# Kernel tuning notes

Measured on AMD Instinct MI355X. Metric: run time of the kernel, lower is better.

Reference implementation:

```python
import jax, jax.numpy as jnp
import numpy as np
from jax.scipy.special import ndtri

BLOCK_SIZE = 32
NF5_OFFSET = 0.9677083  # QLoRA-style tail quantile offset


def _nf5_table():
    # 32-level NormalFloat-5 table: 16 negative levels, zero, 15 positive levels,
    # taken from standard-normal quantiles and normalized so endpoints hit -1 / +1.
    neg = ndtri(jnp.linspace(1.0 - NF5_OFFSET, 0.5, 17))[:-1]   # 16 negative quantiles
    pos = ndtri(jnp.linspace(0.5, NF5_OFFSET, 16))[1:]          # 15 positive quantiles
    neg = neg / (-neg[0])
    pos = pos / pos[-1]
    return jnp.concatenate([neg, jnp.zeros((1,)), pos]).astype(jnp.float32)


def nf5_quantize(x, block_size, table, boundaries):
    # Block-wise NF5 quantization with power-of-2 scales along the last dim.
    shp = x.shape
    xb = x.reshape(-1, block_size)                               # [nblocks, B]
    amax = jnp.max(jnp.abs(xb), axis=1, keepdims=True)
    scale = jnp.exp2(jnp.ceil(jnp.log2(jnp.maximum(amax, 1e-12))))  # power-of-2 scale
    n = xb / scale                                               # normalized to [-1, 1]
    idx = jnp.searchsorted(boundaries, n)                        # nearest-level index
    q = table[idx] * scale                                       # fused dequant
    return q.reshape(shp)


def setup_inputs() -> dict:
    key = jax.random.key(0)
    k1, k2, k3 = jax.random.split(key, 3)
    B, S, Din, Dout = 8, 4096, 1024, 1024
    x = jax.random.normal(k1, (B, S, Din), dtype=jnp.float32)
    # kaiming_uniform_(a=sqrt(5)) -> U(-b, b) with b = sqrt(6/((1+5)*fan_in)) = 1/sqrt(fan_in)
    bound_w = 1.0 / np.sqrt(Din)
    weight = jax.random.uniform(k2, (Dout, Din), minval=-bound_w, maxval=bound_w, dtype=jnp.float32)
    bias = jax.random.uniform(k3, (Dout,), minval=-bound_w, maxval=bound_w, dtype=jnp.float32)
    return {"x": x, "weight": weight, "bias": bias}


def reference(x, weight, bias):
    table = _nf5_table()
    boundaries = (table[:-1] + table[1:]) * 0.5
    qw = nf5_quantize(weight, BLOCK_SIZE, table, boundaries)   # quantize weight along in_features
    qx = nf5_quantize(x, BLOCK_SIZE, table, boundaries)        # quantize_input=True
    # y[b,s,o] = sum_k qx[b,s,k] * qw[o,k] + bias[o]
    y = jnp.einsum('bsk,ok->bso', qx, qw) + bias
    return y
```

## Files before the change

kernel.cpp:

```cpp
#include <hip/hip_runtime.h>
#include <hip/hip_bf16.h>

typedef __attribute__((ext_vector_type(8))) short short8;
typedef __attribute__((ext_vector_type(4))) float f32x4;

struct alignas(16) US8 { unsigned short s[8]; };

__device__ double ndtri_d(double p) {
    const double a1 = -3.969683028665376e+01, a2 = 2.209460984245205e+02,
                 a3 = -2.759285104469687e+02, a4 = 1.383577518672690e+02,
                 a5 = -3.066479806614716e+01, a6 = 2.506628277459239e+00;
    const double b1 = -5.447609879822406e+01, b2 = 1.615858368580409e+02,
                 b3 = -1.556989798598866e+02, b4 = 6.680131188771972e+01,
                 b5 = -1.328068155288572e+01;
    const double c1 = -7.784894002430293e-03, c2 = -3.223964580411365e-01,
                 c3 = -2.400758277161838e+00, c4 = -2.549732539343734e+00,
                 c5 = 4.374664141464968e+00,  c6 = 2.938163982698783e+00;
    const double d1 = 7.784695709041462e-03, d2 = 3.224671290700398e-01,
                 d3 = 2.445134137142996e+00, d4 = 3.754408661907416e+00;
    const double plow = 0.02425, phigh = 1.0 - 0.02425;
    double x;
    if (p < plow) {
        double q = sqrt(-2.0 * log(p));
        x = (((((c1*q+c2)*q+c3)*q+c4)*q+c5)*q+c6) / ((((d1*q+d2)*q+d3)*q+d4)*q+1.0);
    } else if (p <= phigh) {
        double q = p - 0.5, r = q * q;
        x = (((((a1*r+a2)*r+a3)*r+a4)*r+a5)*r+a6)*q / (((((b1*r+b2)*r+b3)*r+b4)*r+b5)*r+1.0);
    } else {
        double q = sqrt(-2.0 * log(1.0 - p));
        x = -(((((c1*q+c2)*q+c3)*q+c4)*q+c5)*q+c6) / ((((d1*q+d2)*q+d3)*q+d4)*q+1.0);
    }
    #pragma unroll
    for (int it = 0; it < 2; ++it) {
        double e = 0.5 * erfc(-x * 0.70710678118654752440) - p;
        double u = e * 2.50662827463100050242 * exp(0.5 * x * x);
        x = x - u / (1.0 + 0.5 * x * u);
    }
    return x;
}

__global__ void build_table_k(float* __restrict__ table, float* __restrict__ bounds,
                              unsigned char* __restrict__ lut) {
    __shared__ float sT[32], sBd[32];
    const int i = threadIdx.x;
    const double OFF = 0.9677083;
    double v;
    if (i == 16) {
        v = 0.0;
    } else if (i < 16) {
        const double a = 1.0 - OFF;
        double p = a + (0.5 - a) * ((double)i / 16.0);
        v = ndtri_d(p) / (-ndtri_d(a));
    } else {
        int j = i - 16;
        double p = 0.5 + (OFF - 0.5) * ((double)j / 15.0);
        v = ndtri_d(p) / ndtri_d(OFF);
    }
    float tv = (float)v;
    sT[i] = tv;
    table[i] = tv;
    __syncthreads();
    float bd;
    if (i < 31) bd = 0.5f * (sT[i] + sT[i + 1]);
    else        bd = __builtin_inff();
    sBd[i] = bd;
    bounds[i] = bd;
    __syncthreads();
    for (int j = i; j < 256; j += 32) {
        float nj = (float)j * (1.0f / 128.0f) - 1.0f - 0x1p-20f;
        int c = 0;
        #pragma unroll
        for (int k = 0; k < 31; ++k) c += (sBd[k] < nj) ? 1 : 0;
        lut[j] = (unsigned char)c;
    }
}

__device__ __forceinline__ unsigned short q_one(float n, float scale,
                                                const float* sT, const float* sBnd,
                                                const unsigned char* sLut) {
    float u = fmaf(n, 0.5f, 0.5f);
    int b = (int)(u * 256.0f);
    b = min(b, 255);
    int base = sLut[b];
    int idx = base + ((sBnd[base] < n) ? 1 : 0);
    float q = sT[idx] * scale;
    __hip_bfloat16 h = __float2bfloat16(q);
    return *reinterpret_cast<unsigned short*>(&h);
}

__global__ __launch_bounds__(256) void quantize_k(const float4* __restrict__ in,
                                                  US8* __restrict__ out,
                                                  const float* __restrict__ table,
                                                  const float* __restrict__ bounds,
                                                  const unsigned char* __restrict__ lut,
                                                  int n8) {
    __shared__ float sT[32], sBnd[32];
    __shared__ unsigned char sLut[256];
    const int tid = threadIdx.x;
    if (tid < 32) { sT[tid] = table[tid]; sBnd[tid] = bounds[tid]; }
    sLut[tid] = lut[tid];
    __syncthreads();
    const int t = blockIdx.x * 256 + tid;
    if (t >= n8) return;
    float4 v0 = in[2 * t];
    float4 v1 = in[2 * t + 1];
    float am = fmaxf(fmaxf(fmaxf(fabsf(v0.x), fabsf(v0.y)), fmaxf(fabsf(v0.z), fabsf(v0.w))),
                     fmaxf(fmaxf(fabsf(v1.x), fabsf(v1.y)), fmaxf(fabsf(v1.z), fabsf(v1.w))));
    am = fmaxf(am, __shfl_xor(am, 1));
    am = fmaxf(am, __shfl_xor(am, 2));
    am = fmaxf(am, 1e-12f);
    int e;
    float m = frexpf(am, &e);
    int se = (m == 0.5f) ? (e - 1) : e;
    float scale = ldexpf(1.0f, se);
    float inv   = ldexpf(1.0f, -se);
    US8 o;
    o.s[0] = q_one(v0.x * inv, scale, sT, sBnd, sLut);
    o.s[1] = q_one(v0.y * inv, scale, sT, sBnd, sLut);
    o.s[2] = q_one(v0.z * inv, scale, sT, sBnd, sLut);
    o.s[3] = q_one(v0.w * inv, scale, sT, sBnd, sLut);
    o.s[4] = q_one(v1.x * inv, scale, sT, sBnd, sLut);
    o.s[5] = q_one(v1.y * inv, scale, sT, sBnd, sLut);
    o.s[6] = q_one(v1.z * inv, scale, sT, sBnd, sLut);
    o.s[7] = q_one(v1.w * inv, scale, sT, sBnd, sLut);
    out[t] = o;
}

__device__ __forceinline__ void gload_lds16(const unsigned short* g, unsigned short* s) {
    __builtin_amdgcn_global_load_lds(
        (const __attribute__((address_space(1))) unsigned int*)g,
        (__attribute__((address_space(3))) unsigned int*)s, 16, 0, 0);
}

__global__ __launch_bounds__(256) void gemm_bt_k(const unsigned short* __restrict__ A,
                                                 const unsigned short* __restrict__ B,
                                                 const float* __restrict__ bias,
                                                 float* __restrict__ C,
                                                 int M, int N, int K) {
    __shared__ unsigned short sA[128 * 64];
    __shared__ unsigned short sB[128 * 64];
    const int t = threadIdx.x;
    const int w = t >> 6, l = t & 63;

    const int nB = N >> 7, mB = M >> 7;
    const unsigned int lin = blockIdx.x;
    int m_idx, n_idx;
    if ((mB & 7) == 0) {
        const unsigned int xcd = lin & 7, seq = lin >> 3;
        n_idx = seq % (unsigned int)nB;
        m_idx = (seq / (unsigned int)nB) * 8 + xcd;
    } else {
        n_idx = lin % (unsigned int)nB;
        m_idx = lin / (unsigned int)nB;
    }
    const int m_blk = m_idx * 128, n_blk = n_idx * 128;
    const int wm = (w >> 1) * 64, wn = (w & 1) * 64;

    f32x4 acc[4][4];
    #pragma unroll
    for (int i = 0; i < 4; ++i)
        #pragma unroll
        for (int j = 0; j < 4; ++j)
            acc[i][j] = (f32x4){0.f, 0.f, 0.f, 0.f};

    const int st_row = (l >> 3);
    const int st_col = (l & 7) * 8;

    for (int kt = 0; kt < K; kt += 64) {
        __syncthreads();
        #pragma unroll
        for (int j = 0; j < 4; ++j) {
            const int chunk = w * 4 + j;
            const int row = chunk * 8 + st_row;
            const unsigned short* ga = A + (size_t)(m_blk + row) * K + kt + st_col;
            const unsigned short* gb = B + (size_t)(n_blk + row) * K + kt + st_col;
            gload_lds16(ga, &sA[chunk * 512]);
            gload_lds16(gb, &sB[chunk * 512]);
        }
        __syncthreads();
        #pragma unroll
        for (int ks = 0; ks < 2; ++ks) {
            const int kof = ks * 32 + (l >> 4) * 8;
            const int rsel = l & 15;
            short8 a[4], b[4];
            #pragma unroll
            for (int i = 0; i < 4; ++i) {
                a[i] = *(const short8*)&sA[(wm + i * 16 + rsel) * 64 + kof];
                b[i] = *(const short8*)&sB[(wn + i * 16 + rsel) * 64 + kof];
            }
            #pragma unroll
            for (int i = 0; i < 4; ++i)
                #pragma unroll
                for (int j = 0; j < 4; ++j)
                    acc[i][j] = __builtin_amdgcn_mfma_f32_16x16x32_bf16(
                        a[i], b[j], acc[i][j], 0, 0, 0);
        }
    }

    float bv[4];
    #pragma unroll
    for (int j = 0; j < 4; ++j) bv[j] = bias[n_blk + wn + j * 16 + (l & 15)];
    #pragma unroll
    for (int i = 0; i < 4; ++i) {
        #pragma unroll
        for (int r = 0; r < 4; ++r) {
            const int row = m_blk + wm + i * 16 + (l >> 4) * 4 + r;
            float* cp = C + (size_t)row * N + n_blk + wn + (l & 15);
            #pragma unroll
            for (int j = 0; j < 4; ++j)
                cp[j * 16] = acc[i][j][r] + bv[j];
        }
    }
}

extern "C" void kernel_launch(void* const* d_in, const int* in_sizes, int n_in,
                              void* d_out, int out_size, void* d_ws, size_t ws_size,
                              hipStream_t stream) {
    const float* x    = (const float*)d_in[0];
    const float* wgt  = (const float*)d_in[1];
    const float* bias = (const float*)d_in[2];
    float* out = (float*)d_out;

    const int x_size = in_sizes[0];
    const int w_size = in_sizes[1];
    const int N = in_sizes[2];
    const int K = w_size / N;
    const int M = x_size / K;

    char* ws = (char*)d_ws;
    unsigned short* qx = (unsigned short*)ws;
    unsigned short* qw = (unsigned short*)(ws + (size_t)M * K * sizeof(unsigned short));
    float* table  = (float*)(ws + (size_t)M * K * 2 + (size_t)N * K * 2);
    float* bounds = table + 32;
    unsigned char* lut = (unsigned char*)(bounds + 32);

    build_table_k<<<1, 32, 0, stream>>>(table, bounds, lut);

    const int n8x = x_size / 8;
    quantize_k<<<(n8x + 255) / 256, 256, 0, stream>>>(
        (const float4*)x, (US8*)qx, table, bounds, lut, n8x);
    const int n8w = w_size / 8;
    quantize_k<<<(n8w + 255) / 256, 256, 0, stream>>>(
        (const float4*)wgt, (US8*)qw, table, bounds, lut, n8w);

    const int grid = (M / 128) * (N / 128);
    gemm_bt_k<<<grid, 256, 0, stream>>>(qx, qw, bias, out, M, N, K);
}
```

Before: 334.7 us.

## Double-buffer GEMM LDS tiles with XOR swizzle and merge quantize launches

The GEMM now keeps two LDS buffers, so the async global-to-LDS load for the next K tile is issued before the MFMA work on the current tile and one barrier per iteration is dropped. LDS columns are XOR-swizzled by row to reduce bank conflicts on the short8 fragment reads. The two quantize launches for input and weight are merged into a single grid that picks its source by block index, removing one launch. LDS use doubles to 64KB per block, which may reduce occupancy.

```diff
diff --git a/kernel.cpp b/kernel.cpp
--- a/kernel.cpp
+++ b/kernel.cpp
@@ -88,19 +88,22 @@
     return *reinterpret_cast<unsigned short*>(&h);
 }
 
-__global__ __launch_bounds__(256) void quantize_k(const float4* __restrict__ in,
-                                                  US8* __restrict__ out,
+__global__ __launch_bounds__(256) void quantize_k(const float4* __restrict__ x,
+                                                  US8* __restrict__ qx, int nblk_x, int n8x,
+                                                  const float4* __restrict__ wgt,
+                                                  US8* __restrict__ qw, int n8w,
                                                   const float* __restrict__ table,
                                                   const float* __restrict__ bounds,
-                                                  const unsigned char* __restrict__ lut,
-                                                  int n8) {
+                                                  const unsigned char* __restrict__ lut) {
     __shared__ float sT[32], sBnd[32];
     __shared__ unsigned char sLut[256];
     const int tid = threadIdx.x;
     if (tid < 32) { sT[tid] = table[tid]; sBnd[tid] = bounds[tid]; }
     sLut[tid] = lut[tid];
     __syncthreads();
-    const int t = blockIdx.x * 256 + tid;
+    const float4* in; US8* out; int t, n8;
+    if ((int)blockIdx.x < nblk_x) { in = x;   out = qx; t = blockIdx.x * 256 + tid;            n8 = n8x; }
+    else                          { in = wgt; out = qw; t = (blockIdx.x - nblk_x) * 256 + tid; n8 = n8w; }
     if (t >= n8) return;
     float4 v0 = in[2 * t];
     float4 v1 = in[2 * t + 1];
@@ -137,8 +140,8 @@
                                                  const float* __restrict__ bias,
                                                  float* __restrict__ C,
                                                  int M, int N, int K) {
-    __shared__ unsigned short sA[128 * 64];
-    __shared__ unsigned short sB[128 * 64];
+    __shared__ unsigned short sA[2][128 * 64];
+    __shared__ unsigned short sB[2][128 * 64];
     const int t = threadIdx.x;
     const int w = t >> 6, l = t & 63;
 
@@ -163,30 +166,43 @@
         for (int j = 0; j < 4; ++j)
             acc[i][j] = (f32x4){0.f, 0.f, 0.f, 0.f};
 
-    const int st_row = (l >> 3);
-    const int st_col = (l & 7) * 8;
-
-    for (int kt = 0; kt < K; kt += 64) {
-        __syncthreads();
+    const int st_row = l >> 3;
+    const int st_col = ((l & 7) ^ st_row) * 8;
+
+    const int kIters = K >> 6;
+
+    auto stage = [&](int buf, int kt) {
         #pragma unroll
         for (int j = 0; j < 4; ++j) {
             const int chunk = w * 4 + j;
             const int row = chunk * 8 + st_row;
             const unsigned short* ga = A + (size_t)(m_blk + row) * K + kt + st_col;
             const unsigned short* gb = B + (size_t)(n_blk + row) * K + kt + st_col;
-            gload_lds16(ga, &sA[chunk * 512]);
-            gload_lds16(gb, &sB[chunk * 512]);
+            gload_lds16(ga, &sA[buf][chunk * 512]);
+            gload_lds16(gb, &sB[buf][chunk * 512]);
         }
+    };
+
+    stage(0, 0);
+
+    const int rsel = l & 15;
+    const int quad = l >> 4;
+    for (int it = 0; it < kIters; ++it) {
         __syncthreads();
+        const int buf = it & 1;
+        if (it + 1 < kIters) stage(buf ^ 1, (it + 1) * 64);
         #pragma unroll
         for (int ks = 0; ks < 2; ++ks) {
-            const int kof = ks * 32 + (l >> 4) * 8;
-            const int rsel = l & 15;
+            const int k8 = ks * 4 + quad;
             short8 a[4], b[4];
             #pragma unroll
             for (int i = 0; i < 4; ++i) {
-                a[i] = *(const short8*)&sA[(wm + i * 16 + rsel) * 64 + kof];
-                b[i] = *(const short8*)&sB[(wn + i * 16 + rsel) * 64 + kof];
+                const int ra = wm + i * 16 + rsel;
+                const int ua = (ra >> 3) * 64 + (ra & 7) * 8 + ((k8 ^ (ra & 7)) & 7);
+                a[i] = *(const short8*)&sA[buf][ua * 8];
+                const int rb = wn + i * 16 + rsel;
+                const int ub = (rb >> 3) * 64 + (rb & 7) * 8 + ((k8 ^ (rb & 7)) & 7);
+                b[i] = *(const short8*)&sB[buf][ub * 8];
             }
             #pragma unroll
             for (int i = 0; i < 4; ++i)
@@ -236,12 +252,11 @@
 
     build_table_k<<<1, 32, 0, stream>>>(table, bounds, lut);
 
-    const int n8x = x_size / 8;
-    quantize_k<<<(n8x + 255) / 256, 256, 0, stream>>>(
-        (const float4*)x, (US8*)qx, table, bounds, lut, n8x);
-    const int n8w = w_size / 8;
-    quantize_k<<<(n8w + 255) / 256, 256, 0, stream>>>(
-        (const float4*)wgt, (US8*)qw, table, bounds, lut, n8w);
+    const int n8x = x_size / 8, n8w = w_size / 8;
+    const int nblk_x = (n8x + 255) / 256, nblk_w = (n8w + 255) / 256;
+    quantize_k<<<nblk_x + nblk_w, 256, 0, stream>>>(
+        (const float4*)x, (US8*)qx, nblk_x, n8x,
+        (const float4*)wgt, (US8*)qw, n8w, table, bounds, lut);
 
     const int grid = (M / 128) * (N / 128);
     gemm_bt_k<<<grid, 256, 0, stream>>>(qx, qw, bias, out, M, N, K);
```

New measurement: 307.7 us. 1.09x faster.
